# Kernel optimization log

Hardware: AMD Instinct MI355X
Metric: run time of the kernel (lower is better)

Reference implementation:

```python
import jax, jax.numpy as jnp
from jax import lax
import numpy as np

INPUT_SIZE = 4
HIDDEN = 64
PROJ = 52


def setup_inputs() -> dict:
    key = jax.random.key(0)
    ks = jax.random.split(key, 6)
    k = 1.0 / np.sqrt(HIDDEN)  # PyTorch LSTM init range
    u = lambda kk, shape: jax.random.uniform(kk, shape, jnp.float32, -k, k)
    return {
        "x": jax.random.normal(ks[0], (4096, 512, INPUT_SIZE), jnp.float32),
        "W_ih": u(ks[1], (4 * HIDDEN, INPUT_SIZE)),   # gates [i,f,g,o]
        "W_hh": u(ks[2], (4 * HIDDEN, PROJ)),          # recurrent acts on projected h
        "b_ih": u(ks[3], (4 * HIDDEN,)),
        "b_hh": u(ks[4], (4 * HIDDEN,)),
        "W_hr": u(ks[5], (PROJ, HIDDEN)),              # projection h = W_hr @ (o*tanh(c))
    }


def reference(x, W_ih, W_hh, b_ih, b_hh, W_hr):
    B = x.shape[0]
    b = b_ih + b_hh
    xT = jnp.swapaxes(x, 0, 1)  # [T, B, input]

    def step(carry, xt):
        h, c = carry  # h: [B, PROJ], c: [B, HIDDEN]
        gates = xt @ W_ih.T + h @ W_hh.T + b  # [B, 4H]
        i, f, g, o = jnp.split(gates, 4, axis=-1)
        i = jax.nn.sigmoid(i)
        f = jax.nn.sigmoid(f)
        g = jnp.tanh(g)
        o = jax.nn.sigmoid(o)
        c = f * c + i * g
        h = (o * jnp.tanh(c)) @ W_hr.T  # projected hidden state
        return (h, c), None

    h0 = jnp.zeros((B, PROJ), x.dtype)
    c0 = jnp.zeros((B, HIDDEN), x.dtype)
    (h_last, _), _ = lax.scan(step, (h0, c0), xT)
    return h_last  # [B, PROJ] == r_out[:, -1, :]
```

## Files before the change

kernel.cpp:

```cpp
#include <hip/hip_runtime.h>


#define T_STEPS 512
#define HID 64
#define NPROJ 52
#define NBATCH 16
#define ROWB 136
#define DBYTES (NBATCH * ROWB)
#define LOG2E 1.44269504088896340736f

typedef _Float16 half8 __attribute__((ext_vector_type(8)));
typedef float f32x4 __attribute__((ext_vector_type(4)));

__device__ __forceinline__ float exp2_f(float x) {
#if __has_builtin(__builtin_amdgcn_exp2f)
    return __builtin_amdgcn_exp2f(x);
#else
    return exp2f(x);
#endif
}
__device__ __forceinline__ float rcp_f(float x) {
    return __builtin_amdgcn_rcpf(x);
}

__global__ __launch_bounds__(256, 1)
void lstmp_kernel(const float* __restrict__ x,
                  const float* __restrict__ Wih,
                  const float* __restrict__ Whh,
                  const float* __restrict__ bih,
                  const float* __restrict__ bhh,
                  const float* __restrict__ Whr,
                  float* __restrict__ out)
{
    __shared__ char dlds[2 * DBYTES];

    const int lane = threadIdx.x & 63;
    const int wave = threadIdx.x >> 6;
    const int quad = lane >> 4;
    const int col  = lane & 15;

    {
        unsigned* ldw = (unsigned*)dlds;
        const int tot = (int)(2 * DBYTES / 4);
        for (int i = threadIdx.x; i < tot; i += 256) ldw[i] = 0u;
    }

    const int hid = wave * 16 + col;
    float macc[4][16];
#pragma unroll
    for (int g = 0; g < 4; ++g)
#pragma unroll
        for (int kk = 0; kk < 16; ++kk) macc[g][kk] = 0.0f;

    for (int p = 0; p < NPROJ; ++p) {
        float wv[4];
#pragma unroll
        for (int g = 0; g < 4; ++g) wv[g] = Whh[(g * HID + hid) * NPROJ + p];
        const float* wr = Whr + p * HID + quad * 8;
        const float4 r0 = *(const float4*)(wr);
        const float4 r1 = *(const float4*)(wr + 4);
        const float4 r2 = *(const float4*)(wr + 32);
        const float4 r3 = *(const float4*)(wr + 36);
        const float rk[16] = {r0.x, r0.y, r0.z, r0.w, r1.x, r1.y, r1.z, r1.w,
                              r2.x, r2.y, r2.z, r2.w, r3.x, r3.y, r3.z, r3.w};
#pragma unroll
        for (int g = 0; g < 4; ++g)
#pragma unroll
            for (int kk = 0; kk < 16; ++kk) macc[g][kk] = fmaf(wv[g], rk[kk], macc[g][kk]);
    }

    half8 aM[4][2];
    half8 aXB[4];
#pragma unroll
    for (int g = 0; g < 4; ++g) {
        const float scale = (g == 2) ? (2.0f * LOG2E) : LOG2E;
#pragma unroll
        for (int ch = 0; ch < 2; ++ch)
#pragma unroll
            for (int j = 0; j < 8; ++j)
                aM[g][ch][j] = (_Float16)(macc[g][ch * 8 + j] * scale);
        const int row = g * HID + hid;
#pragma unroll
        for (int j = 0; j < 8; ++j) {
            const int k = quad * 8 + j;
            float v = 0.0f;
            if (k < 4)       v = Wih[row * 4 + k];
            else if (k == 4) v = bih[row] + bhh[row];
            aXB[g][j] = (_Float16)(v * scale);
        }
    }

    const float4* xp = (const float4*)x + (size_t)blockIdx.x * NBATCH * T_STEPS;
    const float4 xq0 = xp[(size_t)col * T_STEPS + 0];
    float4 xv = xp[(size_t)col * T_STEPS + 1];

    half8 bx;
#pragma unroll
    for (int j = 0; j < 8; ++j) bx[j] = (_Float16)0.0f;
    if (quad == 0) {
        bx[0] = (_Float16)xq0.x; bx[1] = (_Float16)xq0.y;
        bx[2] = (_Float16)xq0.z; bx[3] = (_Float16)xq0.w;
        bx[4] = (_Float16)1.0f;
    }

    float cacc[4] = {0.0f, 0.0f, 0.0f, 0.0f};

    const int dwoff  = col * ROWB + wave * 32 + quad * 8;
    const int drbase = col * ROWB + quad * 16;

    __syncthreads();

#pragma unroll 1
    for (int t = 0; t < T_STEPS; ++t) {
        const char* rbuf = dlds + (t & 1) * DBYTES;
        char* wbuf = dlds + ((t + 1) & 1) * DBYTES;

        f32x4 ai = {0.f,0.f,0.f,0.f}, af_ = {0.f,0.f,0.f,0.f};
        f32x4 ag_ = {0.f,0.f,0.f,0.f}, ao_ = {0.f,0.f,0.f,0.f};
        ai  = __builtin_amdgcn_mfma_f32_16x16x32_f16(aXB[0], bx, ai,  0, 0, 0);
        af_ = __builtin_amdgcn_mfma_f32_16x16x32_f16(aXB[1], bx, af_, 0, 0, 0);
        ag_ = __builtin_amdgcn_mfma_f32_16x16x32_f16(aXB[2], bx, ag_, 0, 0, 0);
        ao_ = __builtin_amdgcn_mfma_f32_16x16x32_f16(aXB[3], bx, ao_, 0, 0, 0);

        half8 bd0, bd1;
        {
            const char* p0 = rbuf + drbase;
            union { unsigned long long q[2]; half8 h; } u0, u1;
            u0.q[0] = *(const unsigned long long*)(p0);
            u0.q[1] = *(const unsigned long long*)(p0 + 8);
            u1.q[0] = *(const unsigned long long*)(p0 + 64);
            u1.q[1] = *(const unsigned long long*)(p0 + 72);
            bd0 = u0.h; bd1 = u1.h;
        }

        half8 bxn;
#pragma unroll
        for (int j = 0; j < 8; ++j) bxn[j] = (_Float16)0.0f;
        if (quad == 0) {
            bxn[0] = (_Float16)xv.x; bxn[1] = (_Float16)xv.y;
            bxn[2] = (_Float16)xv.z; bxn[3] = (_Float16)xv.w;
            bxn[4] = (_Float16)1.0f;
        }
        const int tn = (t + 2 < T_STEPS) ? (t + 2) : (T_STEPS - 1);
        const float4 xnew = xp[(size_t)col * T_STEPS + tn];

        ai  = __builtin_amdgcn_mfma_f32_16x16x32_f16(aM[0][0], bd0, ai,  0, 0, 0);
        af_ = __builtin_amdgcn_mfma_f32_16x16x32_f16(aM[1][0], bd0, af_, 0, 0, 0);
        ag_ = __builtin_amdgcn_mfma_f32_16x16x32_f16(aM[2][0], bd0, ag_, 0, 0, 0);
        ao_ = __builtin_amdgcn_mfma_f32_16x16x32_f16(aM[3][0], bd0, ao_, 0, 0, 0);
        ai  = __builtin_amdgcn_mfma_f32_16x16x32_f16(aM[0][1], bd1, ai,  0, 0, 0);
        af_ = __builtin_amdgcn_mfma_f32_16x16x32_f16(aM[1][1], bd1, af_, 0, 0, 0);
        ag_ = __builtin_amdgcn_mfma_f32_16x16x32_f16(aM[2][1], bd1, ag_, 0, 0, 0);
        ao_ = __builtin_amdgcn_mfma_f32_16x16x32_f16(aM[3][1], bd1, ao_, 0, 0, 0);

        union { _Float16 h[4]; unsigned long long q; } du;
#pragma unroll
        for (int r = 0; r < 4; ++r) {
            const float iv = rcp_f(1.0f + exp2_f(-ai[r]));
            const float fv = rcp_f(1.0f + exp2_f(-af_[r]));
            const float ov = rcp_f(1.0f + exp2_f(-ao_[r]));
            const float gs = fmaf(-4.0f * LOG2E, rcp_f(1.0f + exp2_f(ag_[r])),
                                  2.0f * LOG2E);
            const float cn = fmaf(fv, cacc[r], iv * gs);
            cacc[r] = cn;
            const float th = fmaf(-2.0f, rcp_f(1.0f + exp2_f(cn)), 1.0f);
            du.h[r] = (_Float16)(ov * th);
        }
        *(unsigned long long*)(wbuf + dwoff) = du.q;

        bx = bxn;
        xv = xnew;
        __syncthreads();
    }

    half8 aP[2];
    const int prow = wave * 16 + col;
#pragma unroll
    for (int ch = 0; ch < 2; ++ch)
#pragma unroll
        for (int j = 0; j < 8; ++j) {
            const int k = ch * 32 + quad * 8 + j;
            aP[ch][j] = (_Float16)((prow < NPROJ) ? Whr[prow * HID + k] : 0.0f);
        }

    half8 bd0, bd1;
    {
        const char* p0 = dlds + 0 * DBYTES + drbase;
        union { unsigned long long q[2]; half8 h; } u0, u1;
        u0.q[0] = *(const unsigned long long*)(p0);
        u0.q[1] = *(const unsigned long long*)(p0 + 8);
        u1.q[0] = *(const unsigned long long*)(p0 + 64);
        u1.q[1] = *(const unsigned long long*)(p0 + 72);
        bd0 = u0.h; bd1 = u1.h;
    }
    f32x4 hf = {0.f, 0.f, 0.f, 0.f};
    hf = __builtin_amdgcn_mfma_f32_16x16x32_f16(aP[0], bd0, hf, 0, 0, 0);
    hf = __builtin_amdgcn_mfma_f32_16x16x32_f16(aP[1], bd1, hf, 0, 0, 0);

    const size_t bg = (size_t)blockIdx.x * NBATCH + col;
    float* o = out + bg * NPROJ;
    const int p0 = wave * 16 + quad * 4;
#pragma unroll
    for (int r = 0; r < 4; ++r) {
        const int p = p0 + r;
        if (p < NPROJ) o[p] = hf[r];
    }
}

extern "C" void kernel_launch(void* const* d_in, const int* in_sizes, int n_in,
                              void* d_out, int out_size, void* d_ws, size_t ws_size,
                              hipStream_t stream) {
    const float* x   = (const float*)d_in[0];
    const float* Wih = (const float*)d_in[1];
    const float* Whh = (const float*)d_in[2];
    const float* bih = (const float*)d_in[3];
    const float* bhh = (const float*)d_in[4];
    const float* Whr = (const float*)d_in[5];
    float* out = (float*)d_out;

    dim3 grid(4096 / NBATCH);
    dim3 block(256);
    lstmp_kernel<<<grid, block, 0, stream>>>(x, Wih, Whh, bih, bhh, Whr, out);
}
```

Measured before the change: 310.6 us.

## Ping-pong two wave groups between MFMA and activation stages

Each block now runs 512 threads in two groups of four waves, and each group handles 8 batch rows. While one group runs the gate MFMAs for its batch half, the other runs the transcendental activations, and they swap after every barrier. The MFMA tiles still cover 16 columns, so the gate results are repacked with ds_bpermute so that every lane holds 2 useful outputs instead of 4. This aims to overlap matrix and VALU work across waves on the serial recurrence. The cost is two barriers per step, half the MFMA columns wasted, and extra permute instructions.

New measurement: 463.6 us. 49.2% more time.

```diff
diff --git a/kernel.cpp b/kernel.cpp
--- a/kernel.cpp
+++ b/kernel.cpp
@@ -4,9 +4,8 @@
 #define T_STEPS 512
 #define HID 64
 #define NPROJ 52
-#define NBATCH 16
 #define ROWB 136
-#define DBYTES (NBATCH * ROWB)
+#define GBYTES (16 * ROWB)
 #define LOG2E 1.44269504088896340736f
 
 typedef _Float16 half8 __attribute__((ext_vector_type(8)));
@@ -22,8 +21,11 @@
 __device__ __forceinline__ float rcp_f(float x) {
     return __builtin_amdgcn_rcpf(x);
 }
-
-__global__ __launch_bounds__(256, 1)
+__device__ __forceinline__ float bperm_f(int addrB, float v) {
+    return __int_as_float(__builtin_amdgcn_ds_bpermute(addrB, __float_as_int(v)));
+}
+
+__global__ __launch_bounds__(512, 1)
 void lstmp_kernel(const float* __restrict__ x,
                   const float* __restrict__ Wih,
                   const float* __restrict__ Whh,
@@ -32,20 +34,25 @@
                   const float* __restrict__ Whr,
                   float* __restrict__ out)
 {
-    __shared__ char dlds[2 * DBYTES];
+    __shared__ char dlds[2 * GBYTES];
 
     const int lane = threadIdx.x & 63;
     const int wave = threadIdx.x >> 6;
+    const int grp  = wave >> 2;
+    const int gw   = wave & 3;
     const int quad = lane >> 4;
     const int col  = lane & 15;
+    const bool low = (col & 8) == 0;
+    const int srcB = (lane & ~8) << 2;
+
+    char* dbase = dlds + grp * GBYTES;
 
     {
-        unsigned* ldw = (unsigned*)dlds;
-        const int tot = (int)(2 * DBYTES / 4);
-        for (int i = threadIdx.x; i < tot; i += 256) ldw[i] = 0u;
-    }
-
-    const int hid = wave * 16 + col;
+        unsigned* p = (unsigned*)dlds;
+        for (int i = threadIdx.x; i < (int)(2 * GBYTES / 4); i += 512) p[i] = 0u;
+    }
+
+    const int hid = gw * 16 + col;
     float macc[4][16];
 #pragma unroll
     for (int g = 0; g < 4; ++g)
@@ -90,41 +97,39 @@
         }
     }
 
-    const float4* xp = (const float4*)x + (size_t)blockIdx.x * NBATCH * T_STEPS;
-    const float4 xq0 = xp[(size_t)col * T_STEPS + 0];
-    float4 xv = xp[(size_t)col * T_STEPS + 1];
-
-    half8 bx;
-#pragma unroll
-    for (int j = 0; j < 8; ++j) bx[j] = (_Float16)0.0f;
-    if (quad == 0) {
-        bx[0] = (_Float16)xq0.x; bx[1] = (_Float16)xq0.y;
-        bx[2] = (_Float16)xq0.z; bx[3] = (_Float16)xq0.w;
-        bx[4] = (_Float16)1.0f;
-    }
-
-    float cacc[4] = {0.0f, 0.0f, 0.0f, 0.0f};
-
-    const int dwoff  = col * ROWB + wave * 32 + quad * 8;
+    const int gb = blockIdx.x * 16 + grp * 8 + (col & 7);
+    const float4* xp = (const float4*)x;
+    float4 xcur = xp[(size_t)gb * T_STEPS + 0];
+    float4 xv   = xp[(size_t)gb * T_STEPS + 1];
+    int xi = 2;
+
+    f32x4 ai = {0.f,0.f,0.f,0.f}, af_ = {0.f,0.f,0.f,0.f};
+    f32x4 ag_ = {0.f,0.f,0.f,0.f}, ao_ = {0.f,0.f,0.f,0.f};
+    float cacc[2] = {0.0f, 0.0f};
+
+    const int dwoff  = (col & 7) * ROWB + (16 * gw + quad * 4 + (low ? 0 : 2)) * 2;
     const int drbase = col * ROWB + quad * 16;
 
     __syncthreads();
 
-#pragma unroll 1
-    for (int t = 0; t < T_STEPS; ++t) {
-        const char* rbuf = dlds + (t & 1) * DBYTES;
-        char* wbuf = dlds + ((t + 1) & 1) * DBYTES;
-
-        f32x4 ai = {0.f,0.f,0.f,0.f}, af_ = {0.f,0.f,0.f,0.f};
-        f32x4 ag_ = {0.f,0.f,0.f,0.f}, ao_ = {0.f,0.f,0.f,0.f};
-        ai  = __builtin_amdgcn_mfma_f32_16x16x32_f16(aXB[0], bx, ai,  0, 0, 0);
-        af_ = __builtin_amdgcn_mfma_f32_16x16x32_f16(aXB[1], bx, af_, 0, 0, 0);
-        ag_ = __builtin_amdgcn_mfma_f32_16x16x32_f16(aXB[2], bx, ag_, 0, 0, 0);
-        ao_ = __builtin_amdgcn_mfma_f32_16x16x32_f16(aXB[3], bx, ao_, 0, 0, 0);
+    auto mfma_stage = [&]() {
+        half8 bx;
+#pragma unroll
+        for (int j = 0; j < 8; ++j) bx[j] = (_Float16)0.0f;
+        if (quad == 0) {
+            bx[0] = (_Float16)xcur.x; bx[1] = (_Float16)xcur.y;
+            bx[2] = (_Float16)xcur.z; bx[3] = (_Float16)xcur.w;
+            bx[4] = (_Float16)1.0f;
+        }
+        const f32x4 z = {0.f, 0.f, 0.f, 0.f};
+        ai  = __builtin_amdgcn_mfma_f32_16x16x32_f16(aXB[0], bx, z, 0, 0, 0);
+        af_ = __builtin_amdgcn_mfma_f32_16x16x32_f16(aXB[1], bx, z, 0, 0, 0);
+        ag_ = __builtin_amdgcn_mfma_f32_16x16x32_f16(aXB[2], bx, z, 0, 0, 0);
+        ao_ = __builtin_amdgcn_mfma_f32_16x16x32_f16(aXB[3], bx, z, 0, 0, 0);
 
         half8 bd0, bd1;
         {
-            const char* p0 = rbuf + drbase;
+            const char* p0 = dbase + drbase;
             union { unsigned long long q[2]; half8 h; } u0, u1;
             u0.q[0] = *(const unsigned long long*)(p0);
             u0.q[1] = *(const unsigned long long*)(p0 + 8);
@@ -132,18 +137,6 @@
             u1.q[1] = *(const unsigned long long*)(p0 + 72);
             bd0 = u0.h; bd1 = u1.h;
         }
-
-        half8 bxn;
-#pragma unroll
-        for (int j = 0; j < 8; ++j) bxn[j] = (_Float16)0.0f;
-        if (quad == 0) {
-            bxn[0] = (_Float16)xv.x; bxn[1] = (_Float16)xv.y;
-            bxn[2] = (_Float16)xv.z; bxn[3] = (_Float16)xv.w;
-            bxn[4] = (_Float16)1.0f;
-        }
-        const int tn = (t + 2 < T_STEPS) ? (t + 2) : (T_STEPS - 1);
-        const float4 xnew = xp[(size_t)col * T_STEPS + tn];
-
         ai  = __builtin_amdgcn_mfma_f32_16x16x32_f16(aM[0][0], bd0, ai,  0, 0, 0);
         af_ = __builtin_amdgcn_mfma_f32_16x16x32_f16(aM[1][0], bd0, af_, 0, 0, 0);
         ag_ = __builtin_amdgcn_mfma_f32_16x16x32_f16(aM[2][0], bd0, ag_, 0, 0, 0);
@@ -153,28 +146,53 @@
         ag_ = __builtin_amdgcn_mfma_f32_16x16x32_f16(aM[2][1], bd1, ag_, 0, 0, 0);
         ao_ = __builtin_amdgcn_mfma_f32_16x16x32_f16(aM[3][1], bd1, ao_, 0, 0, 0);
 
-        union { _Float16 h[4]; unsigned long long q; } du;
-#pragma unroll
-        for (int r = 0; r < 4; ++r) {
-            const float iv = rcp_f(1.0f + exp2_f(-ai[r]));
-            const float fv = rcp_f(1.0f + exp2_f(-af_[r]));
-            const float ov = rcp_f(1.0f + exp2_f(-ao_[r]));
-            const float gs = fmaf(-4.0f * LOG2E, rcp_f(1.0f + exp2_f(ag_[r])),
+        xcur = xv;
+        const int tn = (xi < T_STEPS) ? xi : (T_STEPS - 1);
+        xv = xp[(size_t)gb * T_STEPS + tn];
+        ++xi;
+    };
+
+    auto act_stage = [&]() {
+        float yi[2], yf[2], yg[2], yo[2];
+        {
+            const float ti2 = bperm_f(srcB, ai[2]),  ti3 = bperm_f(srcB, ai[3]);
+            const float tf2 = bperm_f(srcB, af_[2]), tf3 = bperm_f(srcB, af_[3]);
+            const float tg2 = bperm_f(srcB, ag_[2]), tg3 = bperm_f(srcB, ag_[3]);
+            const float to2 = bperm_f(srcB, ao_[2]), to3 = bperm_f(srcB, ao_[3]);
+            yi[0] = low ? ai[0]  : ti2;  yi[1] = low ? ai[1]  : ti3;
+            yf[0] = low ? af_[0] : tf2;  yf[1] = low ? af_[1] : tf3;
+            yg[0] = low ? ag_[0] : tg2;  yg[1] = low ? ag_[1] : tg3;
+            yo[0] = low ? ao_[0] : to2;  yo[1] = low ? ao_[1] : to3;
+        }
+        union { _Float16 h[2]; unsigned w; } du;
+#pragma unroll
+        for (int u = 0; u < 2; ++u) {
+            const float iv = rcp_f(1.0f + exp2_f(-yi[u]));
+            const float fv = rcp_f(1.0f + exp2_f(-yf[u]));
+            const float ov = rcp_f(1.0f + exp2_f(-yo[u]));
+            const float gs = fmaf(-4.0f * LOG2E, rcp_f(1.0f + exp2_f(yg[u])),
                                   2.0f * LOG2E);
-            const float cn = fmaf(fv, cacc[r], iv * gs);
-            cacc[r] = cn;
+            const float cn = fmaf(fv, cacc[u], iv * gs);
+            cacc[u] = cn;
             const float th = fmaf(-2.0f, rcp_f(1.0f + exp2_f(cn)), 1.0f);
-            du.h[r] = (_Float16)(ov * th);
-        }
-        *(unsigned long long*)(wbuf + dwoff) = du.q;
-
-        bx = bxn;
-        xv = xnew;
+            du.h[u] = (_Float16)(ov * th);
+        }
+        *(unsigned*)(dbase + dwoff) = du.w;
+    };
+
+    if (grp == 1) mfma_stage();
+    __syncthreads();
+
+#pragma unroll 1
+    for (int t = 0; t < T_STEPS; ++t) {
+        if (grp == 0) mfma_stage(); else act_stage();
         __syncthreads();
+        if (grp == 0) act_stage(); else mfma_stage();
+        __syncthreads();
     }
 
     half8 aP[2];
-    const int prow = wave * 16 + col;
+    const int prow = gw * 16 + col;
 #pragma unroll
     for (int ch = 0; ch < 2; ++ch)
 #pragma unroll
@@ -185,7 +203,7 @@
 
     half8 bd0, bd1;
     {
-        const char* p0 = dlds + 0 * DBYTES + drbase;
+        const char* p0 = dbase + drbase;
         union { unsigned long long q[2]; half8 h; } u0, u1;
         u0.q[0] = *(const unsigned long long*)(p0);
         u0.q[1] = *(const unsigned long long*)(p0 + 8);
@@ -197,13 +215,14 @@
     hf = __builtin_amdgcn_mfma_f32_16x16x32_f16(aP[0], bd0, hf, 0, 0, 0);
     hf = __builtin_amdgcn_mfma_f32_16x16x32_f16(aP[1], bd1, hf, 0, 0, 0);
 
-    const size_t bg = (size_t)blockIdx.x * NBATCH + col;
-    float* o = out + bg * NPROJ;
-    const int p0 = wave * 16 + quad * 4;
-#pragma unroll
-    for (int r = 0; r < 4; ++r) {
-        const int p = p0 + r;
-        if (p < NPROJ) o[p] = hf[r];
+    if (col < 8) {
+        float* o = out + (size_t)gb * NPROJ;
+        const int p0 = gw * 16 + quad * 4;
+#pragma unroll
+        for (int r = 0; r < 4; ++r) {
+            const int p = p0 + r;
+            if (p < NPROJ) o[p] = hf[r];
+        }
     }
 }
 
@@ -218,7 +237,7 @@
     const float* Whr = (const float*)d_in[5];
     float* out = (float*)d_out;
 
-    dim3 grid(4096 / NBATCH);
-    dim3 block(256);
+    dim3 grid(256);
+    dim3 block(512);
     lstmp_kernel<<<grid, block, 0, stream>>>(x, Wih, Whh, bih, bhh, Whr, out);
 }
```
